# Kernel tuning notes

Measured on AMD Instinct MI355X. Metric: run time of the kernel, lower is better.

## Reference

```python
import jax, jax.numpy as jnp
import numpy as np

N = 16384          # total nodes (128 graphs x 128 ops)
G = 128            # number of graphs
NPG = N // G       # nodes per graph
DIN = 64           # op_input_dim
H = 64             # hidden_dim
BN_EPS = 1e-5


def setup_inputs() -> dict:
    key = jax.random.key(0)
    ks = jax.random.split(key, 16)
    x = jax.random.normal(ks[0], (N, DIN), dtype=jnp.float32)
    # sparse-ish 0/1 adjacency stored dense (as torch.mm path expects); add self-loops so degrees > 0
    u = jax.random.uniform(ks[1], (N, N), dtype=jnp.float32)
    adj = jnp.maximum((u < 0.004).astype(jnp.float32), jnp.eye(N, dtype=jnp.float32))
    # graph_pool: [G, N] average-pooling matrix (block rows of 1/NPG)
    rows = jnp.repeat(jnp.arange(G), NPG)
    graph_pool = jnp.zeros((G, N), jnp.float32).at[rows, jnp.arange(N)].set(1.0 / NPG)
    s = 0.05
    params = {}
    dims_in = [DIN, H]
    for l in range(2):
        d_in = dims_in[l]
        params[f"W1_{l}"] = jax.random.normal(ks[2 + 6 * l], (d_in, H), jnp.float32) * s
        params[f"b1_{l}"] = jnp.zeros((H,), jnp.float32)
        params[f"g1_{l}"] = jnp.ones((H,), jnp.float32)
        params[f"be1_{l}"] = jnp.zeros((H,), jnp.float32)
        params[f"W2_{l}"] = jax.random.normal(ks[3 + 6 * l], (H, H), jnp.float32) * s
        params[f"b2_{l}"] = jnp.zeros((H,), jnp.float32)
        params[f"g_{l}"] = jnp.ones((H,), jnp.float32)   # outer BN gamma
        params[f"be_{l}"] = jnp.zeros((H,), jnp.float32)  # outer BN beta
    return {"x": x, "adj": adj, "graph_pool": graph_pool, **params}


def _bn(h, g, b):
    # training-mode BatchNorm1d over node axis (biased var), eps=1e-5
    m = jnp.mean(h, axis=0)
    v = jnp.var(h, axis=0)
    return g * (h - m) * jax.lax.rsqrt(v + BN_EPS) + b


def _mlp(h, W1, b1, g1, be1, W2, b2):
    # 2-layer MLP: Linear -> BN -> ReLU -> Linear
    return jax.nn.relu(_bn(h @ W1 + b1, g1, be1)) @ W2 + b2


def reference(x, adj, graph_pool,
              W1_0, b1_0, g1_0, be1_0, W2_0, b2_0, g_0, be_0,
              W1_1, b1_1, g1_1, be1_1, W2_1, b2_1, g_1, be_1):
    deg = adj @ jnp.ones((adj.shape[0], 1), adj.dtype)  # [N,1]
    h = x
    layers = [
        (W1_0, b1_0, g1_0, be1_0, W2_0, b2_0, g_0, be_0),
        (W1_1, b1_1, g1_1, be1_1, W2_1, b2_1, g_1, be_1),
    ]
    for (W1, b1, g1, be1, W2, b2, g, be) in layers:
        pooled = (adj @ h) / deg                 # average neighbor aggregation
        pooled_rep = _mlp(pooled, W1, b1, g1, be1, W2, b2)
        h = jax.nn.relu(_bn(pooled_rep, g, be))
    h_nodes = h
    pooled_h = graph_pool @ h                    # [G, H] graph readout
    return (pooled_h, h_nodes)
```

## Files before the change

### kernel.cpp

```cpp
#include <hip/hip_runtime.h>
#include <hip/hip_bf16.h>
#include <stdint.h>

#define N_NODES 16384
#define GG      128
#define HD      64
#define MAXD    192
#define BN_EPS  1e-5f

typedef unsigned short u16;
typedef unsigned int   u32;
typedef unsigned long long u64;

__device__ __forceinline__ float bf2f(u16 u) {
    union { u32 i; float f; } c; c.i = ((u32)u) << 16; return c.f;
}
__device__ __forceinline__ float ldp(const void* p, int i, int flag) {
    return flag ? ((const float*)p)[i] : bf2f(((const u16*)p)[i]);
}

__global__ __launch_bounds__(256) void k_init(
    const u32* __restrict__ adj32, double* __restrict__ statsD,
    int* __restrict__ flag)
{
    const int gid = blockIdx.x * 256 + threadIdx.x;
    if (gid < 512) statsD[gid] = 0.0;
    if (gid == 0) *flag = ((adj32[0] & 0xFFFFu) == 0) ? 1 : 0;
}

__global__ __launch_bounds__(256) void k_scan(
    const void* __restrict__ adjv, u16* __restrict__ cols,
    int* __restrict__ cnt, const int* __restrict__ flagp)
{
    const int wave = threadIdx.x >> 6, lane = threadIdx.x & 63;
    const int row = blockIdx.x * 4 + wave;
    u16* __restrict__ crow = cols + (size_t)row * MAXD;
    const int flag = *flagp;
    const u64 ltmask = ((1ull << lane) - 1ull);

    int base = 0;
    if (flag) {
        const u32* __restrict__ arow = (const u32*)adjv + (size_t)row * N_NODES;
        uint4 nxt = *(const uint4*)(arow + lane * 4);
        for (int c = 0; c < N_NODES; c += 256) {
            uint4 raw = nxt;
            if (c + 256 < N_NODES)
                nxt = *(const uint4*)(arow + c + 256 + lane * 4);
            const u32 w[4] = {raw.x, raw.y, raw.z, raw.w};
            #pragma unroll
            for (int e = 0; e < 4; ++e) {
                u64 m = __ballot(w[e] != 0);
                if (m) {
                    if (w[e]) {
                        int p = base + __popcll(m & ltmask);
                        if (p < MAXD) crow[p] = (u16)(c + lane * 4 + e);
                    }
                    base += __popcll(m);
                }
            }
        }
    } else {
        const u16* __restrict__ arow = (const u16*)adjv + (size_t)row * N_NODES;
        uint4 nxt = *(const uint4*)(arow + lane * 8);
        for (int c = 0; c < N_NODES; c += 512) {
            uint4 raw = nxt;
            if (c + 512 < N_NODES)
                nxt = *(const uint4*)(arow + c + 512 + lane * 8);
            const u32 h[4] = {raw.x, raw.y, raw.z, raw.w};
            #pragma unroll
            for (int e = 0; e < 8; ++e) {
                u16 u = (u16)(h[e >> 1] >> ((e & 1) * 16));
                u64 m = __ballot(u != 0);
                if (m) {
                    if (u) {
                        int p = base + __popcll(m & ltmask);
                        if (p < MAXD) crow[p] = (u16)(c + lane * 8 + e);
                    }
                    base += __popcll(m);
                }
            }
        }
    }
    if (lane == 0) cnt[row] = (base < MAXD) ? base : MAXD;
}

__global__ __launch_bounds__(256) void k_gather(
    const void* __restrict__ xv, const u16* __restrict__ cols,
    const int* __restrict__ cnt, float* __restrict__ invdeg,
    float* __restrict__ pooled, const int* __restrict__ flagp)
{
    const int wave = threadIdx.x >> 6, lane = threadIdx.x & 63;
    const int row = blockIdx.x * 4 + wave;
    const int flag = *flagp;
    const u16* __restrict__ crow = cols + (size_t)row * MAXD;
    const int n = cnt[row];
    float acc = 0.f;
    int k = 0;
    if (flag) {
        const float* __restrict__ x = (const float*)xv;
        for (; k + 4 <= n; k += 4) {
            ushort4 j4 = *(const ushort4*)&crow[k];
            float v0 = x[(size_t)j4.x * HD + lane];
            float v1 = x[(size_t)j4.y * HD + lane];
            float v2 = x[(size_t)j4.z * HD + lane];
            float v3 = x[(size_t)j4.w * HD + lane];
            acc += (v0 + v1) + (v2 + v3);
        }
        for (; k < n; ++k) acc += x[(size_t)crow[k] * HD + lane];
    } else {
        const u16* __restrict__ x = (const u16*)xv;
        for (; k + 4 <= n; k += 4) {
            ushort4 j4 = *(const ushort4*)&crow[k];
            float v0 = bf2f(x[(size_t)j4.x * HD + lane]);
            float v1 = bf2f(x[(size_t)j4.y * HD + lane]);
            float v2 = bf2f(x[(size_t)j4.z * HD + lane]);
            float v3 = bf2f(x[(size_t)j4.w * HD + lane]);
            acc += (v0 + v1) + (v2 + v3);
        }
        for (; k < n; ++k) acc += bf2f(x[(size_t)crow[k] * HD + lane]);
    }
    float inv = 1.f / (float)n;
    pooled[(size_t)row * HD + lane] = acc * inv;
    if (lane == 0) invdeg[row] = inv;
}

__global__ __launch_bounds__(256) void k_mm(
    const float* __restrict__ src, const void* __restrict__ W,
    const void* __restrict__ bias, float* __restrict__ dst,
    const int* __restrict__ flagp)
{
    __shared__ float Wf[64 * 64];
    __shared__ float S[4 * 64];
    const int tid = threadIdx.x;
    const int flag = *flagp;
    for (int i = tid; i < 64 * 64; i += 256) Wf[i] = ldp(W, i, flag);
    const int rbase = blockIdx.x * 4;
    S[tid] = src[(size_t)rbase * 64 + tid];
    __syncthreads();
    const int f = tid & 63, r = tid >> 6;
    float acc = ldp(bias, f, flag);
    #pragma unroll
    for (int k = 0; k < 64; ++k)
        acc = fmaf(S[r * 64 + k], Wf[k * 64 + f], acc);
    dst[(size_t)(rbase + r) * 64 + f] = acc;
}

__global__ __launch_bounds__(256) void k_stats(
    const float* __restrict__ src, double* __restrict__ statsOut)
{
    __shared__ double shs[256];
    __shared__ double shq[256];
    const int tid = threadIdx.x;
    const int f = tid & 63, rsub = tid >> 6;
    const int rbase = blockIdx.x * 64;
    double s = 0.0, q = 0.0;
    for (int r = rsub; r < 64; r += 4) {
        float v = src[(size_t)(rbase + r) * 64 + f];
        s += (double)v;
        q += (double)v * (double)v;
    }
    shs[tid] = s; shq[tid] = q;
    __syncthreads();
    if (tid < 64) {
        double S = shs[tid] + shs[64 + tid] + shs[128 + tid] + shs[192 + tid];
        double Q = shq[tid] + shq[64 + tid] + shq[128 + tid] + shq[192 + tid];
        atomicAdd(&statsOut[tid], S);
        atomicAdd(&statsOut[64 + tid], Q);
    }
}

__global__ __launch_bounds__(256) void k_bnrelu(
    const float* __restrict__ src, const double* __restrict__ stats,
    const void* __restrict__ g, const void* __restrict__ be,
    float* __restrict__ dst, const int* __restrict__ flagp)
{
    __shared__ float ac[128];
    const int tid = threadIdx.x;
    const int flag = *flagp;
    if (tid < 64) {
        double m = stats[tid] * (1.0 / N_NODES);
        double v = stats[64 + tid] * (1.0 / N_NODES) - m * m;
        float A = ldp(g, tid, flag) / sqrtf((float)v + BN_EPS);
        ac[tid] = A;
        ac[64 + tid] = ldp(be, tid, flag) - (float)m * A;
    }
    __syncthreads();
    const size_t idx = ((size_t)blockIdx.x * 256 + tid) * 4;
    const int f0 = (int)(idx & 63);
    float4 t = *(const float4*)&src[idx];
    const float4 A4 = *(const float4*)&ac[f0];
    const float4 C4 = *(const float4*)&ac[64 + f0];
    float4 r;
    r.x = fmaxf(fmaf(A4.x, t.x, C4.x), 0.f);
    r.y = fmaxf(fmaf(A4.y, t.y, C4.y), 0.f);
    r.z = fmaxf(fmaf(A4.z, t.z, C4.z), 0.f);
    r.w = fmaxf(fmaf(A4.w, t.w, C4.w), 0.f);
    *(float4*)&dst[idx] = r;
}

__global__ __launch_bounds__(256) void k_spmm(
    const float* __restrict__ h, const u16* __restrict__ cols,
    const int* __restrict__ cnt, const float* __restrict__ invdeg,
    float* __restrict__ pooled)
{
    const int wave = threadIdx.x >> 6, lane = threadIdx.x & 63;
    const int row = blockIdx.x * 4 + wave;
    const u16* __restrict__ crow = cols + (size_t)row * MAXD;
    const int n = cnt[row];
    float acc = 0.f;
    int k = 0;
    for (; k + 4 <= n; k += 4) {
        ushort4 j4 = *(const ushort4*)&crow[k];
        float v0 = h[(size_t)j4.x * HD + lane];
        float v1 = h[(size_t)j4.y * HD + lane];
        float v2 = h[(size_t)j4.z * HD + lane];
        float v3 = h[(size_t)j4.w * HD + lane];
        acc += (v0 + v1) + (v2 + v3);
    }
    for (; k < n; ++k) acc += h[(size_t)crow[k] * HD + lane];
    pooled[(size_t)row * HD + lane] = acc * invdeg[row];
}

__global__ __launch_bounds__(1024) void k_pool(
    const void* __restrict__ gpv, const float* __restrict__ h,
    float* __restrict__ out, const int* __restrict__ flagp)
{
    __shared__ float red[16 * 64];
    const int g = blockIdx.x;
    const int wave = threadIdx.x >> 6, lane = threadIdx.x & 63;
    const int flag = *flagp;
    float acc = 0.f;
    const int jb0 = wave * (N_NODES / 16);
    if (flag) {
        const float* __restrict__ grow = (const float*)gpv + (size_t)g * N_NODES;
        for (int jb = jb0; jb < jb0 + N_NODES / 16; jb += 4) {
            float4 raw = *(const float4*)(grow + jb);
            if (raw.x != 0.f) acc += raw.x * h[(size_t)(jb + 0) * HD + lane];
            if (raw.y != 0.f) acc += raw.y * h[(size_t)(jb + 1) * HD + lane];
            if (raw.z != 0.f) acc += raw.z * h[(size_t)(jb + 2) * HD + lane];
            if (raw.w != 0.f) acc += raw.w * h[(size_t)(jb + 3) * HD + lane];
        }
    } else {
        const u16* __restrict__ grow = (const u16*)gpv + (size_t)g * N_NODES;
        for (int jb = jb0; jb < jb0 + N_NODES / 16; jb += 8) {
            uint4 raw = *(const uint4*)(grow + jb);
            const u32 w[4] = {raw.x, raw.y, raw.z, raw.w};
            #pragma unroll
            for (int e = 0; e < 8; ++e) {
                u16 u = (u16)(w[e >> 1] >> ((e & 1) * 16));
                if (u) acc += bf2f(u) * h[(size_t)(jb + e) * HD + lane];
            }
        }
    }
    red[wave * 64 + lane] = acc;
    __syncthreads();
    if (wave == 0) {
        float s = 0.f;
        #pragma unroll
        for (int w2 = 0; w2 < 16; ++w2) s += red[w2 * 64 + lane];
        out[g * 64 + lane] = s;
    }
}

extern "C" void kernel_launch(void* const* d_in, const int* in_sizes, int n_in,
                              void* d_out, int out_size, void* d_ws, size_t ws_size,
                              hipStream_t stream)
{
    const void* x    = d_in[0];
    const void* adj  = d_in[1];
    const void* gp   = d_in[2];
    const void* W1_0 = d_in[3];
    const void* b1_0 = d_in[4];
    const void* g1_0 = d_in[5];
    const void* be1_0= d_in[6];
    const void* W2_0 = d_in[7];
    const void* b2_0 = d_in[8];
    const void* g_0  = d_in[9];
    const void* be_0 = d_in[10];
    const void* W1_1 = d_in[11];
    const void* b1_1 = d_in[12];
    const void* g1_1 = d_in[13];
    const void* be1_1= d_in[14];
    const void* W2_1 = d_in[15];
    const void* b2_1 = d_in[16];
    const void* g_1  = d_in[17];
    const void* be_1 = d_in[18];

    char* ws = (char*)d_ws;
    float*  P      = (float*) (ws);
    float*  A      = (float*) (ws + (4u  << 20));
    float*  B      = (float*) (ws + (8u  << 20));
    u16*    cols   = (u16*)   (ws + (12u << 20));
    int*    cnt    = (int*)   (ws + (18u << 20));
    float*  invdeg = (float*) (ws + (18u << 20) + 65536);
    double* sd     = (double*)(ws + (18u << 20) + 131072);
    int*    flag   = (int*)   (ws + (18u << 20) + 131072 + 4096);

    float* out_pool  = (float*)d_out;
    float* out_nodes = (float*)d_out + GG * HD;

    const int EB = (N_NODES * HD / 4) / 256;

    k_init<<<2, 256, 0, stream>>>((const u32*)adj, sd, flag);
    k_scan<<<N_NODES / 4, 256, 0, stream>>>(adj, cols, cnt, flag);
    k_gather<<<N_NODES / 4, 256, 0, stream>>>(x, cols, cnt, invdeg, P, flag);

    k_mm<<<N_NODES / 4, 256, 0, stream>>>(P, W1_0, b1_0, A, flag);
    k_stats<<<256, 256, 0, stream>>>(A, sd + 0);
    k_bnrelu<<<EB, 256, 0, stream>>>(A, sd + 0, g1_0, be1_0, B, flag);
    k_mm<<<N_NODES / 4, 256, 0, stream>>>(B, W2_0, b2_0, P, flag);
    k_stats<<<256, 256, 0, stream>>>(P, sd + 128);
    k_bnrelu<<<EB, 256, 0, stream>>>(P, sd + 128, g_0, be_0, A, flag);
    k_spmm<<<N_NODES / 4, 256, 0, stream>>>(A, cols, cnt, invdeg, B);
    k_mm<<<N_NODES / 4, 256, 0, stream>>>(B, W1_1, b1_1, P, flag);
    k_stats<<<256, 256, 0, stream>>>(P, sd + 256);
    k_bnrelu<<<EB, 256, 0, stream>>>(P, sd + 256, g1_1, be1_1, A, flag);
    k_mm<<<N_NODES / 4, 256, 0, stream>>>(A, W2_1, b2_1, B, flag);
    k_stats<<<256, 256, 0, stream>>>(B, sd + 384);
    k_bnrelu<<<EB, 256, 0, stream>>>(B, sd + 384, g_1, be_1, out_nodes, flag);
    k_pool<<<GG, 1024, 0, stream>>>(gp, out_nodes, out_pool, flag);
}
```

Measured before the change: 1.672 ms.

## Fuse BN+ReLU into following matmul/SpMM and deepen nontemporal adjacency scan prefetch

Three separate BN+ReLU kernels are removed. The normalization affine and ReLU are now applied on the fly when the next k_mm loads its input rows, or when k_spmm gathers neighbor features. This saves a full read-write pass over the 16384x64 activation per removed kernel. The adjacency scan now loads two iterations ahead and uses nontemporal loads, so the streamed 1 GB dense matrix should not pollute the cache. In exchange, the BN coefficients are recomputed in every block or wave, and the affine is applied once per gathered neighbor in SpMM.

```diff
diff --git a/kernel.cpp b/kernel.cpp
--- a/kernel.cpp
+++ b/kernel.cpp
@@ -11,6 +11,7 @@
 typedef unsigned short u16;
 typedef unsigned int   u32;
 typedef unsigned long long u64;
+typedef u32 u32x4 __attribute__((ext_vector_type(4)));
 
 __device__ __forceinline__ float bf2f(u16 u) {
     union { u32 i; float f; } c; c.i = ((u32)u) << 16; return c.f;
@@ -40,18 +41,21 @@
 
     int base = 0;
     if (flag) {
-        const u32* __restrict__ arow = (const u32*)adjv + (size_t)row * N_NODES;
-        uint4 nxt = *(const uint4*)(arow + lane * 4);
+        const u32x4* __restrict__ arow =
+            (const u32x4*)((const u32*)adjv + (size_t)row * N_NODES) + lane;
+        u32x4 p0 = __builtin_nontemporal_load(arow);
+        u32x4 p1 = __builtin_nontemporal_load(arow + 64);
         for (int c = 0; c < N_NODES; c += 256) {
-            uint4 raw = nxt;
-            if (c + 256 < N_NODES)
-                nxt = *(const uint4*)(arow + c + 256 + lane * 4);
-            const u32 w[4] = {raw.x, raw.y, raw.z, raw.w};
+            u32x4 raw = p0;
+            p0 = p1;
+            if (c + 512 < N_NODES)
+                p1 = __builtin_nontemporal_load(arow + (c + 512) / 4);
             #pragma unroll
             for (int e = 0; e < 4; ++e) {
-                u64 m = __ballot(w[e] != 0);
+                u32 w = raw[e];
+                u64 m = __ballot(w != 0);
                 if (m) {
-                    if (w[e]) {
+                    if (w) {
                         int p = base + __popcll(m & ltmask);
                         if (p < MAXD) crow[p] = (u16)(c + lane * 4 + e);
                     }
@@ -60,16 +64,18 @@
             }
         }
     } else {
-        const u16* __restrict__ arow = (const u16*)adjv + (size_t)row * N_NODES;
-        uint4 nxt = *(const uint4*)(arow + lane * 8);
+        const u32x4* __restrict__ arow =
+            (const u32x4*)((const u16*)adjv + (size_t)row * N_NODES) + lane;
+        u32x4 p0 = __builtin_nontemporal_load(arow);
+        u32x4 p1 = __builtin_nontemporal_load(arow + 64);
         for (int c = 0; c < N_NODES; c += 512) {
-            uint4 raw = nxt;
-            if (c + 512 < N_NODES)
-                nxt = *(const uint4*)(arow + c + 512 + lane * 8);
-            const u32 h[4] = {raw.x, raw.y, raw.z, raw.w};
+            u32x4 raw = p0;
+            p0 = p1;
+            if (c + 1024 < N_NODES)
+                p1 = __builtin_nontemporal_load(arow + (c + 1024) / 8);
             #pragma unroll
             for (int e = 0; e < 8; ++e) {
-                u16 u = (u16)(h[e >> 1] >> ((e & 1) * 16));
+                u16 u = (u16)(raw[e >> 1] >> ((e & 1) * 16));
                 u64 m = __ballot(u != 0);
                 if (m) {
                     if (u) {
@@ -124,18 +130,35 @@
     if (lane == 0) invdeg[row] = inv;
 }
 
+template<bool AFFINE>
 __global__ __launch_bounds__(256) void k_mm(
-    const float* __restrict__ src, const void* __restrict__ W,
-    const void* __restrict__ bias, float* __restrict__ dst,
-    const int* __restrict__ flagp)
+    const float* __restrict__ src, const double* __restrict__ stats,
+    const void* __restrict__ g, const void* __restrict__ be,
+    const void* __restrict__ W, const void* __restrict__ bias,
+    float* __restrict__ dst, const int* __restrict__ flagp)
 {
     __shared__ float Wf[64 * 64];
     __shared__ float S[4 * 64];
+    __shared__ float ac[128];
     const int tid = threadIdx.x;
     const int flag = *flagp;
+    if (AFFINE) {
+        if (tid < 64) {
+            double m = stats[tid] * (1.0 / N_NODES);
+            double v = stats[64 + tid] * (1.0 / N_NODES) - m * m;
+            float A = ldp(g, tid, flag) / sqrtf((float)v + BN_EPS);
+            ac[tid] = A;
+            ac[64 + tid] = ldp(be, tid, flag) - (float)m * A;
+        }
+        __syncthreads();
+    }
     for (int i = tid; i < 64 * 64; i += 256) Wf[i] = ldp(W, i, flag);
     const int rbase = blockIdx.x * 4;
-    S[tid] = src[(size_t)rbase * 64 + tid];
+    {
+        float v = src[(size_t)rbase * 64 + tid];
+        if (AFFINE) v = fmaxf(fmaf(ac[tid & 63], v, ac[64 + (tid & 63)]), 0.f);
+        S[tid] = v;
+    }
     __syncthreads();
     const int f = tid & 63, r = tid >> 6;
     float acc = ldp(bias, f, flag);
@@ -199,25 +222,39 @@
 }
 
 __global__ __launch_bounds__(256) void k_spmm(
-    const float* __restrict__ h, const u16* __restrict__ cols,
-    const int* __restrict__ cnt, const float* __restrict__ invdeg,
-    float* __restrict__ pooled)
+    const float* __restrict__ t, const double* __restrict__ stats,
+    const void* __restrict__ g, const void* __restrict__ be,
+    const u16* __restrict__ cols, const int* __restrict__ cnt,
+    const float* __restrict__ invdeg, float* __restrict__ pooled,
+    const int* __restrict__ flagp)
 {
     const int wave = threadIdx.x >> 6, lane = threadIdx.x & 63;
     const int row = blockIdx.x * 4 + wave;
+    const int flag = *flagp;
+    double md = stats[lane] * (1.0 / N_NODES);
+    double vd = stats[64 + lane] * (1.0 / N_NODES) - md * md;
+    const float A = ldp(g, lane, flag) / sqrtf((float)vd + BN_EPS);
+    const float C = ldp(be, lane, flag) - (float)md * A;
+
     const u16* __restrict__ crow = cols + (size_t)row * MAXD;
     const int n = cnt[row];
     float acc = 0.f;
     int k = 0;
     for (; k + 4 <= n; k += 4) {
         ushort4 j4 = *(const ushort4*)&crow[k];
-        float v0 = h[(size_t)j4.x * HD + lane];
-        float v1 = h[(size_t)j4.y * HD + lane];
-        float v2 = h[(size_t)j4.z * HD + lane];
-        float v3 = h[(size_t)j4.w * HD + lane];
-        acc += (v0 + v1) + (v2 + v3);
-    }
-    for (; k < n; ++k) acc += h[(size_t)crow[k] * HD + lane];
+        float v0 = t[(size_t)j4.x * HD + lane];
+        float v1 = t[(size_t)j4.y * HD + lane];
+        float v2 = t[(size_t)j4.z * HD + lane];
+        float v3 = t[(size_t)j4.w * HD + lane];
+        acc += fmaxf(fmaf(A, v0, C), 0.f);
+        acc += fmaxf(fmaf(A, v1, C), 0.f);
+        acc += fmaxf(fmaf(A, v2, C), 0.f);
+        acc += fmaxf(fmaf(A, v3, C), 0.f);
+    }
+    for (; k < n; ++k) {
+        float vv = t[(size_t)crow[k] * HD + lane];
+        acc += fmaxf(fmaf(A, vv, C), 0.f);
+    }
     pooled[(size_t)row * HD + lane] = acc * invdeg[row];
 }
 
@@ -305,18 +342,20 @@
     k_scan<<<N_NODES / 4, 256, 0, stream>>>(adj, cols, cnt, flag);
     k_gather<<<N_NODES / 4, 256, 0, stream>>>(x, cols, cnt, invdeg, P, flag);
 
-    k_mm<<<N_NODES / 4, 256, 0, stream>>>(P, W1_0, b1_0, A, flag);
+    k_mm<false><<<N_NODES / 4, 256, 0, stream>>>(P, nullptr, nullptr, nullptr,
+                                                 W1_0, b1_0, A, flag);
     k_stats<<<256, 256, 0, stream>>>(A, sd + 0);
-    k_bnrelu<<<EB, 256, 0, stream>>>(A, sd + 0, g1_0, be1_0, B, flag);
-    k_mm<<<N_NODES / 4, 256, 0, stream>>>(B, W2_0, b2_0, P, flag);
+    k_mm<true><<<N_NODES / 4, 256, 0, stream>>>(A, sd + 0, g1_0, be1_0,
+                                                W2_0, b2_0, P, flag);
     k_stats<<<256, 256, 0, stream>>>(P, sd + 128);
-    k_bnrelu<<<EB, 256, 0, stream>>>(P, sd + 128, g_0, be_0, A, flag);
-    k_spmm<<<N_NODES / 4, 256, 0, stream>>>(A, cols, cnt, invdeg, B);
-    k_mm<<<N_NODES / 4, 256, 0, stream>>>(B, W1_1, b1_1, P, flag);
-    k_stats<<<256, 256, 0, stream>>>(P, sd + 256);
-    k_bnrelu<<<EB, 256, 0, stream>>>(P, sd + 256, g1_1, be1_1, A, flag);
-    k_mm<<<N_NODES / 4, 256, 0, stream>>>(A, W2_1, b2_1, B, flag);
-    k_stats<<<256, 256, 0, stream>>>(B, sd + 384);
-    k_bnrelu<<<EB, 256, 0, stream>>>(B, sd + 384, g_1, be_1, out_nodes, flag);
+    k_spmm<<<N_NODES / 4, 256, 0, stream>>>(P, sd + 128, g_0, be_0,
+                                            cols, cnt, invdeg, B, flag);
+    k_mm<false><<<N_NODES / 4, 256, 0, stream>>>(B, nullptr, nullptr, nullptr,
+                                                 W1_1, b1_1, A, flag);
+    k_stats<<<256, 256, 0, stream>>>(A, sd + 256);
+    k_mm<true><<<N_NODES / 4, 256, 0, stream>>>(A, sd + 256, g1_1, be1_1,
+                                                W2_1, b2_1, P, flag);
+    k_stats<<<256, 256, 0, stream>>>(P, sd + 384);
+    k_bnrelu<<<EB, 256, 0, stream>>>(P, sd + 384, g_1, be_1, out_nodes, flag);
     k_pool<<<GG, 1024, 0, stream>>>(gp, out_nodes, out_pool, flag);
 }
```

New measurement: 1.634 ms. -2.3%, faster.
